# Performance work log

Hardware: AMD Instinct MI355X
Metric: run time of the kernel (lower is better)

## Reference

```python
import jax, jax.numpy as jnp
import numpy as np

N = 50000        # nodes
E = 400000       # edges (avg degree 8)
F_IN = 128       # num_features
HID = 64         # hidden_channels
H = 4            # num_heads
D = HID // H     # headc = 16
C = 16           # num_classes
K_HOPS = 3
ALPHA = 0.1
CST = 1e-5


def setup_inputs() -> dict:
    key = jax.random.key(0)
    ks = jax.random.split(key, 16)
    s = 0.05
    x = jax.random.normal(ks[0], (N, F_IN), dtype=jnp.float32)
    edge_index = jax.random.randint(ks[1], (2, E), 0, N, dtype=jnp.int64)
    Wi = jax.random.normal(ks[2], (F_IN, HID), dtype=jnp.float32) * s
    bi = jnp.zeros((HID,), dtype=jnp.float32)
    Wq = jax.random.normal(ks[3], (HID, H * D), dtype=jnp.float32) * s
    bq = jnp.zeros((H * D,), dtype=jnp.float32)
    Wk = jax.random.normal(ks[4], (HID, H * D), dtype=jnp.float32) * s
    bk = jnp.zeros((H * D,), dtype=jnp.float32)
    Wv = jax.random.normal(ks[5], (HID, H * C), dtype=jnp.float32) * s
    bv = jnp.zeros((H * C,), dtype=jnp.float32)
    Wo = jax.random.normal(ks[6], (H * C, C), dtype=jnp.float32) * s
    bo = jnp.zeros((C,), dtype=jnp.float32)
    # hopwise/temp init as in the torch module (ind_gamma=True, gamma_softmax=True)
    hw = ALPHA * (1.0 - ALPHA) ** np.arange(K_HOPS + 1)
    hw[-1] = (1.0 - ALPHA) ** K_HOPS
    hopwise = jnp.asarray(hw, dtype=jnp.float32)
    temp = jax.random.uniform(ks[7], (H, K_HOPS + 1), dtype=jnp.float32)
    return {"x": x, "edge_index": edge_index, "Wi": Wi, "bi": bi, "Wq": Wq,
            "bq": bq, "Wk": Wk, "bk": bk, "Wv": Wv, "bv": bv, "Wo": Wo,
            "bo": bo, "hopwise": hopwise, "temp": temp}


def reference(x, edge_index, Wi, bi, Wq, bq, Wk, bk, Wv, bv, Wo, bo, hopwise, temp):
    # dropout p=0 (inference); input transform + relu
    h = jax.nn.relu(x @ Wi + bi)                       # (N, HID)
    Q = (1.0 + jax.nn.elu(h @ Wq + bq)).reshape(N, H, D)
    Kt = (1.0 + jax.nn.elu(h @ Wk + bk)).reshape(N, H, D)
    V = (h @ Wv + bv).reshape(N, H, C)
    M = jnp.einsum('nhi,nhj->nhij', Kt, V)             # (N, H, D, C)
    hidden = V * temp[:, 0][None, :, None]             # hop-0 term
    # NB: torch F.softmax(temp, dim=-2) normalizes over the HEAD axis
    layerwise = jax.nn.softmax(temp, axis=0)           # (H, K+1)
    src, dst = edge_index[0], edge_index[1]
    for hop in range(K_HOPS):
        M = jax.ops.segment_sum(M[src], dst, num_segments=N)
        Kt = jax.ops.segment_sum(Kt[src], dst, num_segments=N)
        Hm = jnp.einsum('nhi,nhij->nhj', Q, M)         # (N, H, C)
        den = jnp.einsum('nhi,nhi->nh', Q, Kt)[..., None] + CST
        gamma = hopwise[hop + 1] * layerwise[:, hop + 1][:, None]  # (H, 1)
        hidden = hidden + gamma * (Hm / den)
    # multi_concat=True path
    out = hidden.reshape(N, H * C) @ Wo + bo           # (N, C)
    return out
```

## Files before the change

### kernel.cpp

```cpp
#include <hip/hip_runtime.h>
#include <math.h>

#define F_IN 128
#define HID  64
#define NH   4
#define DD   16
#define CC   16
#define CSTE 1e-5f

typedef _Float16 h2     __attribute__((ext_vector_type(2)));
typedef float    f2     __attribute__((ext_vector_type(2)));
typedef short    short8 __attribute__((ext_vector_type(8)));
typedef float    f4v    __attribute__((ext_vector_type(4)));

#define WIT_LD 136
#define W2T_LD 72
#define H_LD   72

__device__ __forceinline__ unsigned short bf16r(float f) {
    unsigned int u = __builtin_bit_cast(unsigned int, f);
    unsigned int r = (u + 0x7FFFu + ((u >> 16) & 1u)) >> 16;
    return (unsigned short)r;
}

__device__ __forceinline__ int uni(int v) {
    return __builtin_amdgcn_readfirstlane(v);
}

__device__ __forceinline__ float fp8_to_f32(unsigned int b) {
    f2 v = __builtin_amdgcn_cvt_pk_f32_fp8((int)b, false);
    return v.x;
}
__device__ __forceinline__ f2 fp8x2_to_f32(unsigned int w) {
    return __builtin_amdgcn_cvt_pk_f32_fp8((int)w, false);
}
__device__ __forceinline__ unsigned char f32_to_fp8(float f) {
    int w = __builtin_amdgcn_cvt_pk_fp8_f32(f, f, 0, false);
    return (unsigned char)(w & 0xff);
}

__device__ __forceinline__ float fp4_dec1(unsigned int n) {
    unsigned int e = (n >> 1) & 3u, m = n & 1u;
    float mag = (e == 0) ? 0.5f * (float)m
                         : (float)(1u << (e - 1)) * (1.0f + 0.5f * (float)m);
    return (n & 8u) ? -mag : mag;
}
__device__ __forceinline__ unsigned int fp4_enc1(float f) {
    unsigned int s = (f < 0.f) ? 8u : 0u;
    float a = fabsf(f);
    unsigned int m;
    if      (a < 0.25f) m = 0u;
    else if (a < 0.75f) m = 1u;
    else if (a < 1.25f) m = 2u;
    else if (a < 1.75f) m = 3u;
    else if (a < 2.5f)  m = 4u;
    else if (a < 3.5f)  m = 5u;
    else if (a < 5.0f)  m = 6u;
    else                m = 7u;
    return s | m;
}

#if __has_builtin(__builtin_amdgcn_cvt_scalef32_pk_f32_fp4) && __has_builtin(__builtin_amdgcn_cvt_scalef32_pk_fp4_f32)
#define HAS_FP4 1
#endif

__device__ __forceinline__ void fp4x16_dec2(uint2 w, f2* v) {
#ifdef HAS_FP4
    v[0] = __builtin_amdgcn_cvt_scalef32_pk_f32_fp4(w.x, 1.0f, 0);
    v[1] = __builtin_amdgcn_cvt_scalef32_pk_f32_fp4(w.x, 1.0f, 1);
    v[2] = __builtin_amdgcn_cvt_scalef32_pk_f32_fp4(w.x, 1.0f, 2);
    v[3] = __builtin_amdgcn_cvt_scalef32_pk_f32_fp4(w.x, 1.0f, 3);
    v[4] = __builtin_amdgcn_cvt_scalef32_pk_f32_fp4(w.y, 1.0f, 0);
    v[5] = __builtin_amdgcn_cvt_scalef32_pk_f32_fp4(w.y, 1.0f, 1);
    v[6] = __builtin_amdgcn_cvt_scalef32_pk_f32_fp4(w.y, 1.0f, 2);
    v[7] = __builtin_amdgcn_cvt_scalef32_pk_f32_fp4(w.y, 1.0f, 3);
#else
    #pragma unroll
    for (int j = 0; j < 4; ++j) {
        v[j].x     = fp4_dec1((w.x >> (8 * j)) & 0xFu);
        v[j].y     = fp4_dec1((w.x >> (8 * j + 4)) & 0xFu);
        v[4 + j].x = fp4_dec1((w.y >> (8 * j)) & 0xFu);
        v[4 + j].y = fp4_dec1((w.y >> (8 * j + 4)) & 0xFu);
    }
#endif
}

__device__ __forceinline__ uint2 fp4x16_enc(const float* v) {
#ifdef HAS_FP4
    unsigned int a = 0u, b = 0u;
    a = __builtin_amdgcn_cvt_scalef32_pk_fp4_f32(a, v[0],  v[1],  1.0f, 0);
    a = __builtin_amdgcn_cvt_scalef32_pk_fp4_f32(a, v[2],  v[3],  1.0f, 1);
    a = __builtin_amdgcn_cvt_scalef32_pk_fp4_f32(a, v[4],  v[5],  1.0f, 2);
    a = __builtin_amdgcn_cvt_scalef32_pk_fp4_f32(a, v[6],  v[7],  1.0f, 3);
    b = __builtin_amdgcn_cvt_scalef32_pk_fp4_f32(b, v[8],  v[9],  1.0f, 0);
    b = __builtin_amdgcn_cvt_scalef32_pk_fp4_f32(b, v[10], v[11], 1.0f, 1);
    b = __builtin_amdgcn_cvt_scalef32_pk_fp4_f32(b, v[12], v[13], 1.0f, 2);
    b = __builtin_amdgcn_cvt_scalef32_pk_fp4_f32(b, v[14], v[15], 1.0f, 3);
    return {a, b};
#else
    unsigned int a = 0u, b = 0u;
    #pragma unroll
    for (int j = 0; j < 8; ++j) {
        a |= fp4_enc1(v[j])     << (4 * j);
        b |= fp4_enc1(v[8 + j]) << (4 * j);
    }
    return {a, b};
#endif
}

__device__ __forceinline__ void store_m_row(
    uint2* __restrict__ Mout, unsigned short* __restrict__ SKout,
    int node, int lane, const float* u, float kacc)
{
    float rm = 0.f;
    #pragma unroll
    for (int j = 0; j < 16; ++j) rm = fmaxf(rm, fabsf(u[j]));
    unsigned char s8 = f32_to_fp8(rm * (1.0f / 6.0f));
    float se = fp8_to_f32((unsigned int)s8);
    float invs = (se > 0.f) ? (1.0f / se) : 0.f;
    float tq[16];
    #pragma unroll
    for (int j = 0; j < 16; ++j) tq[j] = u[j] * invs;
    Mout[(size_t)node * 64 + lane] = fp4x16_enc(tq);
    SKout[(size_t)node * 64 + lane] =
        (unsigned short)((unsigned short)s8 | ((unsigned short)f32_to_fp8(kacc) << 8));
}

__device__ __forceinline__ float gamma_for(const float* __restrict__ temp,
                                           const float* __restrict__ hopwise,
                                           int h, int hop) {
    float t0 = temp[0 * 4 + hop], t1 = temp[1 * 4 + hop];
    float t2 = temp[2 * 4 + hop], t3 = temp[3 * 4 + hop];
    float mx = fmaxf(fmaxf(t0, t1), fmaxf(t2, t3));
    float e0 = __expf(t0 - mx), e1 = __expf(t1 - mx);
    float e2 = __expf(t2 - mx), e3 = __expf(t3 - mx);
    float ssum = e0 + e1 + e2 + e3;
    float eh = (h == 0) ? e0 : (h == 1) ? e1 : (h == 2) ? e2 : e3;
    return hopwise[hop] * eh / ssum;
}

__device__ __forceinline__ void reduce_scatter16(float* u, int p) {
    #pragma unroll
    for (int k = 0; k < 4; ++k) {
        const int m = 1 << k;
        bool bit = (p >> k) & 1;
        const int n = 8 >> k;
        #pragma unroll
        for (int j = 0; j < n; ++j) {
            float give = bit ? u[2 * j]     : u[2 * j + 1];
            float keep = bit ? u[2 * j + 1] : u[2 * j];
            float got  = __shfl_xor(give, m, 64);
            u[j] = keep + got;
        }
    }
}

__device__ __forceinline__ float den16(float qd, float kacc) {
    float kq = qd * kacc;
    kq += __shfl_xor(kq, 1, 64);
    kq += __shfl_xor(kq, 2, 64);
    kq += __shfl_xor(kq, 4, 64);
    kq += __shfl_xor(kq, 8, 64);
    return kq + CSTE;
}

__device__ __forceinline__ void acc_edge23(f2* u2, float& kacc,
                                           uint2 w, unsigned int skraw) {
    f2 sk = fp8x2_to_f32(skraw);
    kacc += sk.y;
    f2 v[8];
    fp4x16_dec2(w, v);
    f2 s = {sk.x, sk.x};
    #pragma unroll
    for (int j = 0; j < 8; ++j) u2[j] = s * v[j] + u2[j];
}

__device__ __forceinline__ void acc_edge1(h2* u16, float& kacc,
                                          uint4 a0, uint4 a1, unsigned int kraw) {
    float kk = fp8_to_f32(kraw);
    kacc += kk;
    _Float16 kh = (_Float16)kk;
    h2 k2 = {kh, kh};
    const unsigned int aw[8] = {a0.x, a0.y, a0.z, a0.w, a1.x, a1.y, a1.z, a1.w};
    #pragma unroll
    for (int j = 0; j < 8; ++j)
        u16[j] += k2 * __builtin_bit_cast(h2, aw[j]);
}

__global__ __launch_bounds__(1024) void scan_a(const int* __restrict__ deg,
                                               int* __restrict__ offsets,
                                               int* __restrict__ bsum, int N) {
    __shared__ int wsum[16], woff[16];
    int lane = threadIdx.x & 63, w = threadIdx.x >> 6;
    int i0 = blockIdx.x * 4096 + (int)threadIdx.x * 4;
    int d0 = (i0 + 0 < N) ? deg[i0 + 0] : 0;
    int d1 = (i0 + 1 < N) ? deg[i0 + 1] : 0;
    int d2 = (i0 + 2 < N) ? deg[i0 + 2] : 0;
    int d3 = (i0 + 3 < N) ? deg[i0 + 3] : 0;
    int tsum = d0 + d1 + d2 + d3;
    int incl = tsum;
    #pragma unroll
    for (int m = 1; m < 64; m <<= 1) {
        int t = __shfl_up(incl, m, 64);
        if (lane >= m) incl += t;
    }
    if (lane == 63) wsum[w] = incl;
    __syncthreads();
    if (threadIdx.x == 0) {
        int r = 0;
        for (int k = 0; k < 16; ++k) { int t = wsum[k]; woff[k] = r; r += t; }
        bsum[blockIdx.x] = r;
    }
    __syncthreads();
    int excl = woff[w] + incl - tsum;
    if (i0 + 0 < N) offsets[i0 + 0] = excl;
    if (i0 + 1 < N) offsets[i0 + 1] = excl + d0;
    if (i0 + 2 < N) offsets[i0 + 2] = excl + d0 + d1;
    if (i0 + 3 < N) offsets[i0 + 3] = excl + d0 + d1 + d2;
}

__global__ void scan_c(int* __restrict__ offsets, const int* __restrict__ bsum,
                       int nb, int N) {
    int i = blockIdx.x * blockDim.x + threadIdx.x;
    if (i < N) {
        int bkt = i >> 12;
        int base = 0;
        for (int b = 0; b < bkt; ++b) base += bsum[b];
        offsets[i] += base;
    }
    if (i == 0) {
        int tot = 0;
        for (int b = 0; b < nb; ++b) tot += bsum[b];
        offsets[N] = tot;
    }
}

__global__ void scatter_kernel(const int* __restrict__ ei, const int* __restrict__ offsets,
                               int* __restrict__ cursor, int* __restrict__ csr, int E) {
    int e = blockIdx.x * blockDim.x + threadIdx.x;
    if (e < E) {
        int src = ei[e];
        int dst = ei[E + e];
        int pos = atomicAdd(&cursor[dst], 1);
        csr[offsets[dst] + pos] = src;
    }
}

__global__ __launch_bounds__(256) void qkv_count(
    const float* __restrict__ x,
    const float* __restrict__ Wi, const float* __restrict__ bi,
    const float* __restrict__ Wq, const float* __restrict__ bq,
    const float* __restrict__ Wk, const float* __restrict__ bk,
    const float* __restrict__ Wv, const float* __restrict__ bv,
    float* __restrict__ Q, unsigned char* __restrict__ K0,
    _Float16* __restrict__ Vh,
    const int* __restrict__ ei, int* __restrict__ deg,
    int E, int qb, int N)
{
    __shared__ unsigned short wit[64 * WIT_LD];
    __shared__ unsigned short w2t[192 * W2T_LD];
    __shared__ unsigned short hlds[64 * H_LD];
    if ((int)blockIdx.x >= qb) {
        int e = ((int)blockIdx.x - qb) * 256 + (int)threadIdx.x;
        if (e < E) atomicAdd(&deg[ei[E + e]], 1);
        return;
    }
    int t = threadIdx.x;
    #pragma unroll
    for (int i = 0; i < 32; ++i) {
        int g = t + i * 256;
        wit[(g & 63) * WIT_LD + (g >> 6)] = bf16r(Wi[g]);
    }
    #pragma unroll
    for (int i = 0; i < 16; ++i) {
        int g = t + i * 256;
        int k = g >> 6, n = g & 63;
        w2t[(n      ) * W2T_LD + k] = bf16r(Wq[g]);
        w2t[(n +  64) * W2T_LD + k] = bf16r(Wk[g]);
        w2t[(n + 128) * W2T_LD + k] = bf16r(Wv[g]);
    }
    __syncthreads();

    int lane = t & 63, w = t >> 6;
    int p = lane & 15, quad = lane >> 4;
    int mbase = blockIdx.x * 64 + w * 16;

    short8 afrag[4];
    {
        int node = mbase + p;
        if (node >= N) node = N - 1;
        const float* xr = x + (size_t)node * F_IN + quad * 8;
        #pragma unroll
        for (int ks = 0; ks < 4; ++ks) {
            float4 a0 = *(const float4*)(xr + ks * 32);
            float4 a1 = *(const float4*)(xr + ks * 32 + 4);
            short8 f;
            f[0] = bf16r(a0.x); f[1] = bf16r(a0.y); f[2] = bf16r(a0.z); f[3] = bf16r(a0.w);
            f[4] = bf16r(a1.x); f[5] = bf16r(a1.y); f[6] = bf16r(a1.z); f[7] = bf16r(a1.w);
            afrag[ks] = f;
        }
    }
    #pragma unroll
    for (int nt = 0; nt < 4; ++nt) {
        f4v acc = {0.f, 0.f, 0.f, 0.f};
        #pragma unroll
        for (int ks = 0; ks < 4; ++ks) {
            short8 b = *(const short8*)&wit[(nt * 16 + p) * WIT_LD + ks * 32 + quad * 8];
            acc = __builtin_amdgcn_mfma_f32_16x16x32_bf16(afrag[ks], b, acc, 0, 0, 0);
        }
        float bb = bi[nt * 16 + p];
        #pragma unroll
        for (int r = 0; r < 4; ++r) {
            float hv = fmaxf(acc[r] + bb, 0.f);
            hlds[(w * 16 + quad * 4 + r) * H_LD + nt * 16 + p] = bf16r(hv);
        }
    }
    __syncthreads();

    short8 ha0 = *(const short8*)&hlds[(w * 16 + p) * H_LD + quad * 8];
    short8 ha1 = *(const short8*)&hlds[(w * 16 + p) * H_LD + 32 + quad * 8];
    int node_r = mbase + quad * 4;
    #pragma unroll
    for (int nt = 0; nt < 12; ++nt) {
        f4v acc = {0.f, 0.f, 0.f, 0.f};
        short8 b0 = *(const short8*)&w2t[(nt * 16 + p) * W2T_LD + quad * 8];
        short8 b1 = *(const short8*)&w2t[(nt * 16 + p) * W2T_LD + 32 + quad * 8];
        acc = __builtin_amdgcn_mfma_f32_16x16x32_bf16(ha0, b0, acc, 0, 0, 0);
        acc = __builtin_amdgcn_mfma_f32_16x16x32_bf16(ha1, b1, acc, 0, 0, 0);
        int col = nt * 16 + p;
        #pragma unroll
        for (int r = 0; r < 4; ++r) {
            int node = node_r + r;
            if (node >= N) continue;
            float v = acc[r];
            if (col < 64) {
                v += bq[col];
                Q[(size_t)node * 64 + col] = (v > 0.f) ? (1.f + v) : __expf(v);
            } else if (col < 128) {
                int c = col - 64;
                v += bk[c];
                float kv = (v > 0.f) ? (1.f + v) : __expf(v);
                K0[(size_t)node * 64 + c] = f32_to_fp8(kv);
            } else {
                int c = col - 128;
                v += bv[c];
                Vh[(size_t)node * 64 + c] = (_Float16)v;
            }
        }
    }
}


__global__ __launch_bounds__(256) void hop1_all(
    const float* __restrict__ Q, const unsigned char* __restrict__ K0,
    const _Float16* __restrict__ Vh,
    const int* __restrict__ offsets, const int* __restrict__ csr,
    const float* __restrict__ temp, const float* __restrict__ hopwise,
    uint2* __restrict__ M1, unsigned short* __restrict__ SK1,
    float* __restrict__ hidden, int N)
{
    int lane = threadIdx.x & 63;
    int node = blockIdx.x * 4 + (threadIdx.x >> 6);
    if (node >= N) return;
    int h = lane >> 4;
    float gh = gamma_for(temp, hopwise, h, 1);
    float h0 = (float)Vh[(size_t)node * 64 + lane] * temp[h * 4];
    float qd = Q[(size_t)node * 64 + lane];
    h2 u16[8];
    #pragma unroll
    for (int j = 0; j < 8; ++j) u16[j] = h2{(_Float16)0.f, (_Float16)0.f};
    float kacc = 0.f;
    int beg = uni(offsets[node]), end = uni(offsets[node + 1]);
    int t = beg;
    for (; t + 3 < end; t += 4) {
        int s0 = uni(csr[t]),     s1 = uni(csr[t + 1]);
        int s2 = uni(csr[t + 2]), s3 = uni(csr[t + 3]);
        const uint4* v0p = (const uint4*)(Vh + (size_t)s0 * 64 + h * 16);
        const uint4* v1p = (const uint4*)(Vh + (size_t)s1 * 64 + h * 16);
        const uint4* v2p = (const uint4*)(Vh + (size_t)s2 * 64 + h * 16);
        const uint4* v3p = (const uint4*)(Vh + (size_t)s3 * 64 + h * 16);
        uint4 a00 = v0p[0], a01 = v0p[1];
        uint4 a10 = v1p[0], a11 = v1p[1];
        uint4 a20 = v2p[0], a21 = v2p[1];
        uint4 a30 = v3p[0], a31 = v3p[1];
        unsigned char k0 = K0[(size_t)s0 * 64 + lane];
        unsigned char k1 = K0[(size_t)s1 * 64 + lane];
        unsigned char k2 = K0[(size_t)s2 * 64 + lane];
        unsigned char k3 = K0[(size_t)s3 * 64 + lane];
        acc_edge1(u16, kacc, a00, a01, k0);
        acc_edge1(u16, kacc, a10, a11, k1);
        acc_edge1(u16, kacc, a20, a21, k2);
        acc_edge1(u16, kacc, a30, a31, k3);
    }
    for (; t < end; ++t) {
        int s = uni(csr[t]);
        const uint4* vp = (const uint4*)(Vh + (size_t)s * 64 + h * 16);
        uint4 a0 = vp[0], a1 = vp[1];
        unsigned char kk = K0[(size_t)s * 64 + lane];
        acc_edge1(u16, kacc, a0, a1, kk);
    }
    float u[16];
    #pragma unroll
    for (int j = 0; j < 8; ++j) { u[2 * j] = (float)u16[j].x; u[2 * j + 1] = (float)u16[j].y; }
    store_m_row(M1, SK1, node, lane, u, kacc);
    #pragma unroll
    for (int j = 0; j < 16; ++j) u[j] *= qd;
    reduce_scatter16(u, lane & 15);
    float g = gh / den16(qd, kacc);
    hidden[(size_t)node * 64 + lane] = h0 + g * u[0];
}

template<bool STORE>
__global__ __launch_bounds__(256) void hop23_all(
    const float* __restrict__ Q, const uint2* __restrict__ Mprev,
    const unsigned short* __restrict__ SKprev,
    const int* __restrict__ offsets, const int* __restrict__ csr,
    const float* __restrict__ temp, const float* __restrict__ hopwise,
    uint2* __restrict__ Mnext, unsigned short* __restrict__ SKnext,
    float* __restrict__ hidden,
    const float* __restrict__ Wo, const float* __restrict__ bo,
    float* __restrict__ out, int N, int hop)
{
    int lane = threadIdx.x & 63;
    int node = blockIdx.x * 4 + (threadIdx.x >> 6);
    if (node >= N) return;
    float gh = gamma_for(temp, hopwise, lane >> 4, hop);
    float qd  = Q[(size_t)node * 64 + lane];
    float hv0 = STORE ? 0.f : hidden[(size_t)node * 64 + lane];
    f2 u2[8];
    #pragma unroll
    for (int j = 0; j < 8; ++j) u2[j] = f2{0.f, 0.f};
    float kacc = 0.f;
    int beg = uni(offsets[node]), end = uni(offsets[node + 1]);
    int t = beg;
    for (; t + 7 < end; t += 8) {
        int s[8];
        #pragma unroll
        for (int i = 0; i < 8; ++i) s[i] = uni(csr[t + i]);
        uint2 w[8];
        unsigned short skr[8];
        #pragma unroll
        for (int i = 0; i < 8; ++i) {
            w[i]   = Mprev[(size_t)s[i] * 64 + lane];
            skr[i] = SKprev[(size_t)s[i] * 64 + lane];
        }
        #pragma unroll
        for (int i = 0; i < 8; ++i) acc_edge23(u2, kacc, w[i], skr[i]);
    }
    for (; t + 3 < end; t += 4) {
        int s[4];
        #pragma unroll
        for (int i = 0; i < 4; ++i) s[i] = uni(csr[t + i]);
        uint2 w[4];
        unsigned short skr[4];
        #pragma unroll
        for (int i = 0; i < 4; ++i) {
            w[i]   = Mprev[(size_t)s[i] * 64 + lane];
            skr[i] = SKprev[(size_t)s[i] * 64 + lane];
        }
        #pragma unroll
        for (int i = 0; i < 4; ++i) acc_edge23(u2, kacc, w[i], skr[i]);
    }
    for (; t < end; ++t) {
        int sn = uni(csr[t]);
        uint2 w = Mprev[(size_t)sn * 64 + lane];
        unsigned short skr = SKprev[(size_t)sn * 64 + lane];
        acc_edge23(u2, kacc, w, skr);
    }
    float u[16];
    #pragma unroll
    for (int j = 0; j < 8; ++j) { u[2 * j] = u2[j].x; u[2 * j + 1] = u2[j].y; }
    if constexpr (STORE) store_m_row(Mnext, SKnext, node, lane, u, kacc);
    #pragma unroll
    for (int j = 0; j < 16; ++j) u[j] *= qd;
    reduce_scatter16(u, lane & 15);
    float g = gh / den16(qd, kacc);
    if constexpr (STORE) {
        hidden[(size_t)node * 64 + lane] += g * u[0];
    } else {
        float wrow[16];
        {
            const f4v* wp = (const f4v*)(Wo + (size_t)lane * 16);
            f4v a = wp[0], b = wp[1], c = wp[2], d = wp[3];
            wrow[0]=a[0]; wrow[1]=a[1]; wrow[2]=a[2]; wrow[3]=a[3];
            wrow[4]=b[0]; wrow[5]=b[1]; wrow[6]=b[2]; wrow[7]=b[3];
            wrow[8]=c[0]; wrow[9]=c[1]; wrow[10]=c[2]; wrow[11]=c[3];
            wrow[12]=d[0]; wrow[13]=d[1]; wrow[14]=d[2]; wrow[15]=d[3];
        }
        float hv = hv0 + g * u[0];
        float o[16];
        #pragma unroll
        for (int j = 0; j < 16; ++j) o[j] = hv * wrow[j];
        reduce_scatter16(o, lane & 15);
        float r = o[0];
        r += __shfl_xor(r, 16, 64);
        r += __shfl_xor(r, 32, 64);
        if (lane < 16) out[(size_t)node * 16 + lane] = r + bo[lane];
    }
}

extern "C" void kernel_launch(void* const* d_in, const int* in_sizes, int n_in,
                              void* d_out, int out_size, void* d_ws, size_t ws_size,
                              hipStream_t stream) {
    const float* x       = (const float*)d_in[0];
    const int*   ei      = (const int*)  d_in[1];
    const float* Wi      = (const float*)d_in[2];
    const float* bi      = (const float*)d_in[3];
    const float* Wq      = (const float*)d_in[4];
    const float* bq      = (const float*)d_in[5];
    const float* Wk      = (const float*)d_in[6];
    const float* bk      = (const float*)d_in[7];
    const float* Wv      = (const float*)d_in[8];
    const float* bv      = (const float*)d_in[9];
    const float* Wo      = (const float*)d_in[10];
    const float* bo      = (const float*)d_in[11];
    const float* hopwise = (const float*)d_in[12];
    const float* temp    = (const float*)d_in[13];

    const int N = in_sizes[0] / F_IN;
    const int E = in_sizes[1] / 2;

    char* ws = (char*)d_ws;
    size_t off = 0;
    auto take = [&](size_t bytes) -> char* {
        char* p = ws + off;
        off += (bytes + 255) & ~(size_t)255;
        return p;
    };
    float*          Q      = (float*)take((size_t)N * 64 * 4);
    _Float16*       Vh     = (_Float16*)take((size_t)N * 64 * 2);
    float*          hidden = (float*)take((size_t)N * 64 * 4);
    unsigned char*  K0     = (unsigned char*)take((size_t)N * 64);
    unsigned short* SK1    = (unsigned short*)take((size_t)N * 64 * 2);
    unsigned short* SK2    = (unsigned short*)take((size_t)N * 64 * 2);
    int*            degcur = (int*)take((size_t)2 * N * 4);
    int*            offs   = (int*)take((size_t)(N + 1) * 4);
    int*            csr    = (int*)take((size_t)E * 4);
    int             nb     = (N + 4095) / 4096;
    int*            bsum   = (int*)take((size_t)nb * 4);
    uint2*          M1     = (uint2*)take((size_t)N * 512);
    uint2*          M2     = (uint2*)take((size_t)N * 512);

    int* deg    = degcur;
    int* cursor = degcur + N;

    hipMemsetAsync(degcur, 0, (size_t)2 * N * 4, stream);

    int eb = (E + 255) / 256;
    int qb = (N + 63) / 64;
    qkv_count<<<qb + eb, 256, 0, stream>>>(x, Wi, bi, Wq, bq, Wk, bk, Wv, bv,
                                           Q, K0, Vh,
                                           ei, deg, E, qb, N);
    scan_a<<<nb, 1024, 0, stream>>>(deg, offs, bsum, N);
    scan_c<<<(N + 255) / 256, 256, 0, stream>>>(offs, bsum, nb, N);
    scatter_kernel<<<eb, 256, 0, stream>>>(ei, offs, cursor, csr, E);

    int nb4 = (N + 3) / 4;
    hop1_all<<<nb4, 256, 0, stream>>>(Q, K0, Vh, offs, csr, temp, hopwise,
                                      M1, SK1, hidden, N);
    hop23_all<true ><<<nb4, 256, 0, stream>>>(Q, M1, SK1, offs, csr, temp, hopwise,
                                              M2, SK2, hidden,
                                              (const float*)nullptr, (const float*)nullptr,
                                              (float*)nullptr, N, 2);
    hop23_all<false><<<nb4, 256, 0, stream>>>(Q, M2, SK2, offs, csr, temp, hopwise,
                                              (uint2*)nullptr, (unsigned short*)nullptr,
                                              hidden, Wo, bo, (float*)d_out, N, 3);
}
```

Before: 298.1 us.

## Interleave FP4 M rows and scale/K bytes into one 12-byte record per lane

```diff
diff --git a/kernel.cpp b/kernel.cpp
--- a/kernel.cpp
+++ b/kernel.cpp
@@ -64,23 +64,23 @@
 #define HAS_FP4 1
 #endif
 
-__device__ __forceinline__ void fp4x16_dec2(uint2 w, f2* v) {
+__device__ __forceinline__ void fp4x16_dec2(unsigned int wx, unsigned int wy, f2* v) {
 #ifdef HAS_FP4
-    v[0] = __builtin_amdgcn_cvt_scalef32_pk_f32_fp4(w.x, 1.0f, 0);
-    v[1] = __builtin_amdgcn_cvt_scalef32_pk_f32_fp4(w.x, 1.0f, 1);
-    v[2] = __builtin_amdgcn_cvt_scalef32_pk_f32_fp4(w.x, 1.0f, 2);
-    v[3] = __builtin_amdgcn_cvt_scalef32_pk_f32_fp4(w.x, 1.0f, 3);
-    v[4] = __builtin_amdgcn_cvt_scalef32_pk_f32_fp4(w.y, 1.0f, 0);
-    v[5] = __builtin_amdgcn_cvt_scalef32_pk_f32_fp4(w.y, 1.0f, 1);
-    v[6] = __builtin_amdgcn_cvt_scalef32_pk_f32_fp4(w.y, 1.0f, 2);
-    v[7] = __builtin_amdgcn_cvt_scalef32_pk_f32_fp4(w.y, 1.0f, 3);
+    v[0] = __builtin_amdgcn_cvt_scalef32_pk_f32_fp4(wx, 1.0f, 0);
+    v[1] = __builtin_amdgcn_cvt_scalef32_pk_f32_fp4(wx, 1.0f, 1);
+    v[2] = __builtin_amdgcn_cvt_scalef32_pk_f32_fp4(wx, 1.0f, 2);
+    v[3] = __builtin_amdgcn_cvt_scalef32_pk_f32_fp4(wx, 1.0f, 3);
+    v[4] = __builtin_amdgcn_cvt_scalef32_pk_f32_fp4(wy, 1.0f, 0);
+    v[5] = __builtin_amdgcn_cvt_scalef32_pk_f32_fp4(wy, 1.0f, 1);
+    v[6] = __builtin_amdgcn_cvt_scalef32_pk_f32_fp4(wy, 1.0f, 2);
+    v[7] = __builtin_amdgcn_cvt_scalef32_pk_f32_fp4(wy, 1.0f, 3);
 #else
     #pragma unroll
     for (int j = 0; j < 4; ++j) {
-        v[j].x     = fp4_dec1((w.x >> (8 * j)) & 0xFu);
-        v[j].y     = fp4_dec1((w.x >> (8 * j + 4)) & 0xFu);
-        v[4 + j].x = fp4_dec1((w.y >> (8 * j)) & 0xFu);
-        v[4 + j].y = fp4_dec1((w.y >> (8 * j + 4)) & 0xFu);
+        v[j].x     = fp4_dec1((wx >> (8 * j)) & 0xFu);
+        v[j].y     = fp4_dec1((wx >> (8 * j + 4)) & 0xFu);
+        v[4 + j].x = fp4_dec1((wy >> (8 * j)) & 0xFu);
+        v[4 + j].y = fp4_dec1((wy >> (8 * j + 4)) & 0xFu);
     }
 #endif
 }
@@ -109,8 +109,7 @@
 }
 
 __device__ __forceinline__ void store_m_row(
-    uint2* __restrict__ Mout, unsigned short* __restrict__ SKout,
-    int node, int lane, const float* u, float kacc)
+    uint3* __restrict__ rec, int node, int lane, const float* u, float kacc)
 {
     float rm = 0.f;
     #pragma unroll
@@ -121,9 +120,9 @@
     float tq[16];
     #pragma unroll
     for (int j = 0; j < 16; ++j) tq[j] = u[j] * invs;
-    Mout[(size_t)node * 64 + lane] = fp4x16_enc(tq);
-    SKout[(size_t)node * 64 + lane] =
-        (unsigned short)((unsigned short)s8 | ((unsigned short)f32_to_fp8(kacc) << 8));
+    uint2 enc = fp4x16_enc(tq);
+    unsigned int sk = (unsigned int)s8 | ((unsigned int)f32_to_fp8(kacc) << 8);
+    rec[(size_t)node * 64 + lane] = {enc.x, enc.y, sk};
 }
 
 __device__ __forceinline__ float gamma_for(const float* __restrict__ temp,
@@ -164,12 +163,11 @@
     return kq + CSTE;
 }
 
-__device__ __forceinline__ void acc_edge23(f2* u2, float& kacc,
-                                           uint2 w, unsigned int skraw) {
-    f2 sk = fp8x2_to_f32(skraw);
+__device__ __forceinline__ void acc_edge23(f2* u2, float& kacc, uint3 w) {
+    f2 sk = fp8x2_to_f32(w.z);
     kacc += sk.y;
     f2 v[8];
-    fp4x16_dec2(w, v);
+    fp4x16_dec2(w.x, w.y, v);
     f2 s = {sk.x, sk.x};
     #pragma unroll
     for (int j = 0; j < 8; ++j) u2[j] = s * v[j] + u2[j];
@@ -350,14 +348,12 @@
     }
 }
 
-
 __global__ __launch_bounds__(256) void hop1_all(
     const float* __restrict__ Q, const unsigned char* __restrict__ K0,
     const _Float16* __restrict__ Vh,
     const int* __restrict__ offsets, const int* __restrict__ csr,
     const float* __restrict__ temp, const float* __restrict__ hopwise,
-    uint2* __restrict__ M1, unsigned short* __restrict__ SK1,
-    float* __restrict__ hidden, int N)
+    uint3* __restrict__ rec1, float* __restrict__ hidden, int N)
 {
     int lane = threadIdx.x & 63;
     int node = blockIdx.x * 4 + (threadIdx.x >> 6);
@@ -402,7 +398,7 @@
     float u[16];
     #pragma unroll
     for (int j = 0; j < 8; ++j) { u[2 * j] = (float)u16[j].x; u[2 * j + 1] = (float)u16[j].y; }
-    store_m_row(M1, SK1, node, lane, u, kacc);
+    store_m_row(rec1, node, lane, u, kacc);
     #pragma unroll
     for (int j = 0; j < 16; ++j) u[j] *= qd;
     reduce_scatter16(u, lane & 15);
@@ -412,12 +408,10 @@
 
 template<bool STORE>
 __global__ __launch_bounds__(256) void hop23_all(
-    const float* __restrict__ Q, const uint2* __restrict__ Mprev,
-    const unsigned short* __restrict__ SKprev,
+    const float* __restrict__ Q, const uint3* __restrict__ recp,
     const int* __restrict__ offsets, const int* __restrict__ csr,
     const float* __restrict__ temp, const float* __restrict__ hopwise,
-    uint2* __restrict__ Mnext, unsigned short* __restrict__ SKnext,
-    float* __restrict__ hidden,
+    uint3* __restrict__ recn, float* __restrict__ hidden,
     const float* __restrict__ Wo, const float* __restrict__ bo,
     float* __restrict__ out, int N, int hop)
 {
@@ -433,44 +427,27 @@
     float kacc = 0.f;
     int beg = uni(offsets[node]), end = uni(offsets[node + 1]);
     int t = beg;
-    for (; t + 7 < end; t += 8) {
-        int s[8];
-        #pragma unroll
-        for (int i = 0; i < 8; ++i) s[i] = uni(csr[t + i]);
-        uint2 w[8];
-        unsigned short skr[8];
-        #pragma unroll
-        for (int i = 0; i < 8; ++i) {
-            w[i]   = Mprev[(size_t)s[i] * 64 + lane];
-            skr[i] = SKprev[(size_t)s[i] * 64 + lane];
-        }
-        #pragma unroll
-        for (int i = 0; i < 8; ++i) acc_edge23(u2, kacc, w[i], skr[i]);
-    }
     for (; t + 3 < end; t += 4) {
-        int s[4];
-        #pragma unroll
-        for (int i = 0; i < 4; ++i) s[i] = uni(csr[t + i]);
-        uint2 w[4];
-        unsigned short skr[4];
-        #pragma unroll
-        for (int i = 0; i < 4; ++i) {
-            w[i]   = Mprev[(size_t)s[i] * 64 + lane];
-            skr[i] = SKprev[(size_t)s[i] * 64 + lane];
-        }
-        #pragma unroll
-        for (int i = 0; i < 4; ++i) acc_edge23(u2, kacc, w[i], skr[i]);
+        int s0 = uni(csr[t]),     s1 = uni(csr[t + 1]);
+        int s2 = uni(csr[t + 2]), s3 = uni(csr[t + 3]);
+        uint3 w0 = recp[(size_t)s0 * 64 + lane];
+        uint3 w1 = recp[(size_t)s1 * 64 + lane];
+        uint3 w2 = recp[(size_t)s2 * 64 + lane];
+        uint3 w3 = recp[(size_t)s3 * 64 + lane];
+        acc_edge23(u2, kacc, w0);
+        acc_edge23(u2, kacc, w1);
+        acc_edge23(u2, kacc, w2);
+        acc_edge23(u2, kacc, w3);
     }
     for (; t < end; ++t) {
         int sn = uni(csr[t]);
-        uint2 w = Mprev[(size_t)sn * 64 + lane];
-        unsigned short skr = SKprev[(size_t)sn * 64 + lane];
-        acc_edge23(u2, kacc, w, skr);
+        uint3 w = recp[(size_t)sn * 64 + lane];
+        acc_edge23(u2, kacc, w);
     }
     float u[16];
     #pragma unroll
     for (int j = 0; j < 8; ++j) { u[2 * j] = u2[j].x; u[2 * j + 1] = u2[j].y; }
-    if constexpr (STORE) store_m_row(Mnext, SKnext, node, lane, u, kacc);
+    if constexpr (STORE) store_m_row(recn, node, lane, u, kacc);
     #pragma unroll
     for (int j = 0; j < 16; ++j) u[j] *= qd;
     reduce_scatter16(u, lane & 15);
@@ -531,15 +508,13 @@
     _Float16*       Vh     = (_Float16*)take((size_t)N * 64 * 2);
     float*          hidden = (float*)take((size_t)N * 64 * 4);
     unsigned char*  K0     = (unsigned char*)take((size_t)N * 64);
-    unsigned short* SK1    = (unsigned short*)take((size_t)N * 64 * 2);
-    unsigned short* SK2    = (unsigned short*)take((size_t)N * 64 * 2);
     int*            degcur = (int*)take((size_t)2 * N * 4);
     int*            offs   = (int*)take((size_t)(N + 1) * 4);
     int*            csr    = (int*)take((size_t)E * 4);
     int             nb     = (N + 4095) / 4096;
     int*            bsum   = (int*)take((size_t)nb * 4);
-    uint2*          M1     = (uint2*)take((size_t)N * 512);
-    uint2*          M2     = (uint2*)take((size_t)N * 512);
+    uint3*          rec1   = (uint3*)take((size_t)N * 64 * 12);
+    uint3*          rec2   = (uint3*)take((size_t)N * 64 * 12);
 
     int* deg    = degcur;
     int* cursor = degcur + N;
@@ -557,12 +532,12 @@
 
     int nb4 = (N + 3) / 4;
     hop1_all<<<nb4, 256, 0, stream>>>(Q, K0, Vh, offs, csr, temp, hopwise,
-                                      M1, SK1, hidden, N);
-    hop23_all<true ><<<nb4, 256, 0, stream>>>(Q, M1, SK1, offs, csr, temp, hopwise,
-                                              M2, SK2, hidden,
+                                      rec1, hidden, N);
+    hop23_all<true ><<<nb4, 256, 0, stream>>>(Q, rec1, offs, csr, temp, hopwise,
+                                              rec2, hidden,
                                               (const float*)nullptr, (const float*)nullptr,
                                               (float*)nullptr, N, 2);
-    hop23_all<false><<<nb4, 256, 0, stream>>>(Q, M2, SK2, offs, csr, temp, hopwise,
-                                              (uint2*)nullptr, (unsigned short*)nullptr,
-                                              hidden, Wo, bo, (float*)d_out, N, 3);
-}
+    hop23_all<false><<<nb4, 256, 0, stream>>>(Q, rec2, offs, csr, temp, hopwise,
+                                              (uint3*)nullptr, hidden,
+                                              Wo, bo, (float*)d_out, N, 3);
+}
```

Result: no change. 296.0 us (-0.7%).
